# Kernel optimization log

Measured on AMD Instinct MI355X. Metric: run time of the kernel, lower is better.

## Reference

```python
import jax, jax.numpy as jnp
import numpy as np

EPS = 1e-5
K = 20
THRESH = 0.5

def _bn_relu(x, g, b, m, v):
    # eval-mode BatchNorm1d followed by ReLU
    return jax.nn.relu(g * (x - m) * jax.lax.rsqrt(v + EPS) + b)

def setup_inputs() -> dict:
    key = jax.random.key(0)
    ks = jax.random.split(key, 16)
    T, C, CI, E, NC = 16384, 256, 8, 5, 13
    B, N = 2, T // 2
    inp = {
        "f_sem": jax.random.normal(ks[0], (T, C), jnp.float32),
        "f_ins": jax.random.normal(ks[1], (T, CI), jnp.float32),
        # equal-size, sorted batch assignment (2 clouds of 8192 points)
        "batch": jnp.repeat(jnp.arange(B, dtype=jnp.int64), N),
        # semantic_adaptation_fc: Linear(C,C) + BN + ReLU
        "W_sem": jax.random.normal(ks[2], (C, C), jnp.float32) * (1.0 / np.sqrt(C)),
        "b_sem": jnp.zeros((C,), jnp.float32),
        "g_sem": jnp.ones((C,), jnp.float32),
        "beta_sem": jnp.zeros((C,), jnp.float32),
        "m_sem": jax.random.normal(ks[3], (C,), jnp.float32) * 0.1,
        "v_sem": jax.random.uniform(ks[4], (C,), jnp.float32, 0.5, 1.5),
        # inst_fc: Linear(8,C) + BN + ReLU
        "W_ins": jax.random.normal(ks[5], (CI, C), jnp.float32) * (1.0 / np.sqrt(CI)),
        "b_ins": jnp.zeros((C,), jnp.float32),
        "g_ins": jnp.ones((C,), jnp.float32),
        "beta_ins": jnp.zeros((C,), jnp.float32),
        "m_ins": jax.random.normal(ks[6], (C,), jnp.float32) * 0.1,
        "v_ins": jax.random.uniform(ks[7], (C,), jnp.float32, 0.5, 1.5),
        # instance_embedding_fc: plain Linear(C,E)
        "W_emb": jax.random.normal(ks[8], (C, E), jnp.float32) * (1.0 / np.sqrt(C)),
        "b_emb": jnp.zeros((E,), jnp.float32),
        # classifier_fc: plain Linear(C,NC)
        "W_cls": jax.random.normal(ks[9], (C, NC), jnp.float32) * (1.0 / np.sqrt(C)),
        "b_cls": jnp.zeros((NC,), jnp.float32),
    }
    return inp

def _instance_fusion(e_ins, f_sem, batch):
    # assumes sorted batch with equal-size segments (enforced by setup_inputs)
    T, C = f_sem.shape
    B = int(batch[-1]) + 1
    N = T // B
    e = e_ins.reshape(B, N, -1)
    f = f_sem.reshape(B, N, C)
    # squared Euclidean pairwise distances per cloud: [B, N, N]
    sq = jnp.sum(e * e, axis=-1)
    d2 = sq[:, :, None] + sq[:, None, :] - 2.0 * jnp.einsum("bnd,bmd->bnm", e, e)
    d2 = jnp.maximum(d2, 0.0)
    neg_vals, idx = jax.lax.top_k(-d2, K)          # k smallest distances, [B,N,K]
    within = (-neg_vals) <= THRESH * THRESH        # distance <= threshold
    self_idx = jnp.broadcast_to(jnp.arange(N)[None, :, None], idx.shape)
    col = jnp.where(within, idx, self_idx)         # fall back to self outside threshold
    neigh = jax.vmap(lambda fb, cb: fb[cb])(f, col)  # [B,N,K,C]
    return jnp.max(neigh, axis=2).reshape(T, C)      # scatter-max == max over neighbors

def reference(f_sem, f_ins, batch,
              W_sem, b_sem, g_sem, beta_sem, m_sem, v_sem,
              W_ins, b_ins, g_ins, beta_ins, m_ins, v_ins,
              W_emb, b_emb, W_cls, b_cls):
    f_sem_prime = _bn_relu(f_sem @ W_sem + b_sem, g_sem, beta_sem, m_sem, v_sem)
    f_ins_h = _bn_relu(f_ins @ W_ins + b_ins, g_ins, beta_ins, m_ins, v_ins)
    f_sins = f_ins_h + f_sem_prime
    e_ins = f_sins @ W_emb + b_emb
    f_isem = _instance_fusion(e_ins, f_sem, batch)
    p_sem = f_isem @ W_cls + b_cls
    return (p_sem, e_ins)
```

## Files before the change

kernel.cpp:

```cpp
#include <hip/hip_runtime.h>
#include <math.h>

#define T 16384
#define C 256
#define CI 8
#define EDIM 5
#define NC 13
#define NPTS 8192
#define KNN 20
#define CAP 128
#define FR 32
#define FRPB 8

typedef float f4v __attribute__((ext_vector_type(4)));
typedef _Float16 h8 __attribute__((ext_vector_type(8)));

__global__ __launch_bounds__(256) void front_kernel(
    const float* __restrict__ f_sem, const float* __restrict__ f_ins,
    const float* __restrict__ W_sem, const float* __restrict__ b_sem,
    const float* __restrict__ g_sem, const float* __restrict__ beta_sem,
    const float* __restrict__ m_sem, const float* __restrict__ v_sem,
    const float* __restrict__ W_ins, const float* __restrict__ b_ins,
    const float* __restrict__ g_ins, const float* __restrict__ beta_ins,
    const float* __restrict__ m_ins, const float* __restrict__ v_ins,
    const float* __restrict__ W_emb, const float* __restrict__ b_emb,
    float* __restrict__ eA, double* __restrict__ eD,
    float* __restrict__ out_e)
{
    __shared__ __align__(16) _Float16 sAh[FR][264];
    __shared__ __align__(16) _Float16 sAl[FR][264];
    __shared__ float bnA1[C], bnB1[C], bnA2[C], bnB2[C];
    __shared__ float weL[C][EDIM];
    __shared__ float lfi[FR][CI];
    __shared__ float sP[4][FR][EDIM];

    const int tid = threadIdx.x;
    const int rowBase = blockIdx.x * FR;

    #pragma unroll
    for (int i = 0; i < 8; i++) {
        const int idx = tid + 256 * i;
        const int g = idx * 4;
        const int row = g >> 8, k = g & 255;
        const float4 v = *(const float4*)(f_sem + (size_t)rowBase * C + g);
        const float vv[4] = {v.x, v.y, v.z, v.w};
        #pragma unroll
        for (int q = 0; q < 4; q++) {
            const _Float16 h = (_Float16)vv[q];
            sAh[row][k + q] = h;
            sAl[row][k + q] = (_Float16)(vv[q] - (float)h);
        }
    }
    {
        const int c = tid;
        const float rs1 = 1.0f / sqrtf(v_sem[c] + 1e-5f);
        const float A1 = g_sem[c] * rs1;
        bnA1[c] = A1;
        bnB1[c] = A1 * (b_sem[c] - m_sem[c]) + beta_sem[c];
        const float rs2 = 1.0f / sqrtf(v_ins[c] + 1e-5f);
        const float A2 = g_ins[c] * rs2;
        bnA2[c] = A2;
        bnB2[c] = A2 * (b_ins[c] - m_ins[c]) + beta_ins[c];
        #pragma unroll
        for (int j = 0; j < EDIM; j++) weL[c][j] = W_emb[c * EDIM + j];
    }
    if (tid < FR * CI) lfi[tid >> 3][tid & 7] = f_ins[rowBase * CI + tid];
    __syncthreads();

    const int w = tid >> 6, lane = tid & 63;
    const int r16 = lane & 15, kq = lane >> 4;
    const int n0 = 64 * w;

    f4v acc[2][4];
    #pragma unroll
    for (int mi = 0; mi < 2; mi++)
        #pragma unroll
        for (int ni = 0; ni < 4; ni++) acc[mi][ni] = (f4v){0.f, 0.f, 0.f, 0.f};

    for (int kt = 0; kt < 8; kt++) {
        const int koff = 32 * kt + 8 * kq;
        const h8 ah0 = *(const h8*)&sAh[r16][koff];
        const h8 ah1 = *(const h8*)&sAh[r16 + 16][koff];
        const h8 al0 = *(const h8*)&sAl[r16][koff];
        const h8 al1 = *(const h8*)&sAl[r16 + 16][koff];
        #pragma unroll
        for (int ni = 0; ni < 4; ni++) {
            const float* wp = W_sem + (size_t)koff * C + (n0 + 16 * ni + r16);
            float wf[8];
            #pragma unroll
            for (int j = 0; j < 8; j++) wf[j] = wp[(size_t)j * C];
            h8 bh, bl;
            #pragma unroll
            for (int j = 0; j < 8; j++) {
                const _Float16 h = (_Float16)wf[j];
                bh[j] = h;
                bl[j] = (_Float16)(wf[j] - (float)h);
            }
            acc[0][ni] = __builtin_amdgcn_mfma_f32_16x16x32_f16(ah0, bh, acc[0][ni], 0, 0, 0);
            acc[1][ni] = __builtin_amdgcn_mfma_f32_16x16x32_f16(ah1, bh, acc[1][ni], 0, 0, 0);
            acc[0][ni] = __builtin_amdgcn_mfma_f32_16x16x32_f16(al0, bh, acc[0][ni], 0, 0, 0);
            acc[1][ni] = __builtin_amdgcn_mfma_f32_16x16x32_f16(al1, bh, acc[1][ni], 0, 0, 0);
            acc[0][ni] = __builtin_amdgcn_mfma_f32_16x16x32_f16(ah0, bl, acc[0][ni], 0, 0, 0);
            acc[1][ni] = __builtin_amdgcn_mfma_f32_16x16x32_f16(ah1, bl, acc[1][ni], 0, 0, 0);
        }
    }

    f4v prow, pcol;
    {
        const f4v z = {0.f, 0.f, 0.f, 0.f};
        h8 ra, rb, ca, cb;
        #pragma unroll
        for (int j = 0; j < 8; j++) {
            ra[j] = (_Float16)(float)r16;
            rb[j] = (_Float16)((kq == 0 && j == 0) ? 1.0f : 0.0f);
            ca[j] = rb[j];
            cb[j] = ra[j];
        }
        prow = __builtin_amdgcn_mfma_f32_16x16x32_f16(ra, rb, z, 0, 0, 0);
        pcol = __builtin_amdgcn_mfma_f32_16x16x32_f16(ca, cb, z, 0, 0, 0);
    }
    const int colm = (int)pcol[0];
    int rloc[4];
    #pragma unroll
    for (int r = 0; r < 4; r++) rloc[r] = (int)prow[r];

    float p[2][4][EDIM];
    #pragma unroll
    for (int mi = 0; mi < 2; mi++)
        #pragma unroll
        for (int r = 0; r < 4; r++)
            #pragma unroll
            for (int j = 0; j < EDIM; j++) p[mi][r][j] = 0.f;

    #pragma unroll
    for (int ni = 0; ni < 4; ni++) {
        const int c = n0 + 16 * ni + colm;
        const float A1 = bnA1[c], B1 = bnB1[c];
        const float A2 = bnA2[c], B2 = bnB2[c];
        float wi[CI], we[EDIM];
        #pragma unroll
        for (int k = 0; k < CI; k++) wi[k] = W_ins[k * C + c];
        #pragma unroll
        for (int j = 0; j < EDIM; j++) we[j] = weL[c][j];
        #pragma unroll
        for (int mi = 0; mi < 2; mi++)
            #pragma unroll
            for (int r = 0; r < 4; r++) {
                const int row = 16 * mi + rloc[r];
                float x2 = 0.f;
                #pragma unroll
                for (int k = 0; k < CI; k++) x2 = fmaf(lfi[row][k], wi[k], x2);
                const float h1 = fmaxf(fmaf(A1, acc[mi][ni][r], B1), 0.f);
                const float h2 = fmaxf(fmaf(A2, x2, B2), 0.f);
                const float s = h1 + h2;
                #pragma unroll
                for (int j = 0; j < EDIM; j++) p[mi][r][j] = fmaf(s, we[j], p[mi][r][j]);
            }
    }

    #pragma unroll
    for (int off = 1; off < 16; off <<= 1)
        #pragma unroll
        for (int mi = 0; mi < 2; mi++)
            #pragma unroll
            for (int r = 0; r < 4; r++)
                #pragma unroll
                for (int j = 0; j < EDIM; j++)
                    p[mi][r][j] += __shfl_xor(p[mi][r][j], off);

    if (r16 == 0) {
        #pragma unroll
        for (int mi = 0; mi < 2; mi++)
            #pragma unroll
            for (int r = 0; r < 4; r++)
                #pragma unroll
                for (int j = 0; j < EDIM; j++)
                    sP[w][16 * mi + rloc[r]][j] = p[mi][r][j];
    }
    __syncthreads();

    if (tid < FR) {
        const int row = rowBase + tid;
        double sq = 0.0;
        #pragma unroll
        for (int j = 0; j < EDIM; j++) {
            const float s = ((sP[0][tid][j] + sP[1][tid][j]) +
                             (sP[2][tid][j] + sP[3][tid][j])) + b_emb[j];
            const double ed = (double)s;
            eD[(size_t)row * 8 + j] = ed;
            sq = fma(ed, ed, sq);
            eA[(size_t)row * 8 + j] = s;
            out_e[(size_t)row * EDIM + j] = s;
        }
        eD[(size_t)row * 8 + 5] = sq;
        eA[(size_t)row * 8 + 5] = (float)sq;
        eA[(size_t)row * 8 + 6] = 0.f;
        eA[(size_t)row * 8 + 7] = 0.f;
    }
}

__global__ __launch_bounds__(256) void stream_kernel(
    const float* __restrict__ eA,
    unsigned short* __restrict__ gcand, int* __restrict__ gcnt)
{
    __shared__ float rA[FRPB][8];
    __shared__ unsigned short cidx[FRPB][CAP];
    __shared__ int cntS[FRPB];

    const int tid = threadIdx.x;
    const int rowBase = blockIdx.x * FRPB;

    if (tid < FRPB * 8) rA[tid >> 3][tid & 7] = eA[(rowBase + (tid >> 3)) * 8 + (tid & 7)];
    if (tid < FRPB) cntS[tid] = 0;
    __syncthreads();

    const int wave = tid >> 6, lane = tid & 63;
    const int cbase = (rowBase >= NPTS) ? NPTS : 0;

    float re[FRPB][5], thrb[FRPB];
    #pragma unroll
    for (int r = 0; r < FRPB; r++) {
        #pragma unroll
        for (int q = 0; q < 5; q++) re[r][q] = rA[r][q];
        thrb[r] = (rA[r][5] - 0.251f) * 0.5f;
    }

    const int cstart = wave * (NPTS / 4);
    for (int cb = cstart; cb < cstart + NPTS / 4; cb += 128) {
        const int j0 = cbase + cb + lane;
        const float4 ea0 = *(const float4*)(eA + (size_t)j0 * 8);
        const float2 eb0 = *(const float2*)(eA + (size_t)j0 * 8 + 4);
        const float4 ea1 = *(const float4*)(eA + (size_t)(j0 + 64) * 8);
        const float2 eb1 = *(const float2*)(eA + (size_t)(j0 + 64) * 8 + 4);
        const float hs0 = 0.5f * eb0.y, hs1 = 0.5f * eb1.y;
        #pragma unroll
        for (int r = 0; r < FRPB; r++) {
            float dot = re[r][0] * ea0.x;
            dot = fmaf(re[r][1], ea0.y, dot); dot = fmaf(re[r][2], ea0.z, dot);
            dot = fmaf(re[r][3], ea0.w, dot); dot = fmaf(re[r][4], eb0.x, dot);
            const bool rec = dot >= (thrb[r] + hs0);
            const unsigned long long m = __ballot(rec);
            if (m) {
                int base;
                if (lane == 0) base = atomicAdd(&cntS[r], (int)__popcll(m));
                base = __shfl(base, 0);
                const int pre = __builtin_amdgcn_mbcnt_hi(
                    (unsigned int)(m >> 32),
                    __builtin_amdgcn_mbcnt_lo((unsigned int)m, 0u));
                const int pos = base + pre;
                if (rec && pos < CAP) cidx[r][pos] = (unsigned short)(cb + lane);
            }
        }
        #pragma unroll
        for (int r = 0; r < FRPB; r++) {
            float dot = re[r][0] * ea1.x;
            dot = fmaf(re[r][1], ea1.y, dot); dot = fmaf(re[r][2], ea1.z, dot);
            dot = fmaf(re[r][3], ea1.w, dot); dot = fmaf(re[r][4], eb1.x, dot);
            const bool rec = dot >= (thrb[r] + hs1);
            const unsigned long long m = __ballot(rec);
            if (m) {
                int base;
                if (lane == 0) base = atomicAdd(&cntS[r], (int)__popcll(m));
                base = __shfl(base, 0);
                const int pre = __builtin_amdgcn_mbcnt_hi(
                    (unsigned int)(m >> 32),
                    __builtin_amdgcn_mbcnt_lo((unsigned int)m, 0u));
                const int pos = base + pre;
                if (rec && pos < CAP) cidx[r][pos] = (unsigned short)(cb + 64 + lane);
            }
        }
    }
    __syncthreads();

    {
        const unsigned int* src = (const unsigned int*)cidx;
        unsigned int* dst = (unsigned int*)(gcand + (size_t)rowBase * CAP);
        dst[tid] = src[tid];
        dst[tid + 256] = src[tid + 256];
        if (tid < FRPB) gcnt[rowBase + tid] = cntS[tid];
    }
}

__device__ __attribute__((noinline)) float4 rescan_topk(
    const float* __restrict__ eA, const float* __restrict__ f_sem,
    const float* __restrict__ reRow, int cbase, int lane)
{
    float re0 = reRow[0], re1 = reRow[1], re2 = reRow[2];
    float re3 = reRow[3], re4 = reRow[4], sqF = reRow[5];
    float4 mx = make_float4(-3.4e38f, -3.4e38f, -3.4e38f, -3.4e38f);
    long long last = -1;
    for (int sel = 0; sel < KNN; sel++) {
        long long best = 0x7fffffffffffffffLL;
        for (int cb = 0; cb < NPTS; cb += 64) {
            const int j = cbase + cb + lane;
            const float4 ea = *(const float4*)(eA + (size_t)j * 8);
            const float2 eb = *(const float2*)(eA + (size_t)j * 8 + 4);
            float dot = re0 * ea.x;
            dot = fmaf(re1, ea.y, dot); dot = fmaf(re2, ea.z, dot);
            dot = fmaf(re3, ea.w, dot); dot = fmaf(re4, eb.x, dot);
            const float d2 = fmaxf((sqF + eb.y) - 2.f * dot, 0.f);
            long long key = (((long long)__float_as_uint(d2)) << 32)
                            | (unsigned int)(cb + lane);
            if (key <= last) key = 0x7fffffffffffffffLL;
            if (key < best) best = key;
        }
        #pragma unroll
        for (int off = 32; off; off >>= 1) {
            const long long o = __shfl_xor(best, off);
            if (o < best) best = o;
        }
        last = best;
        const int idx = (int)(best & 0xffffffffLL);
        const float4 fv = *(const float4*)(f_sem + (size_t)(cbase + idx) * C + lane * 4);
        mx.x = fmaxf(mx.x, fv.x); mx.y = fmaxf(mx.y, fv.y);
        mx.z = fmaxf(mx.z, fv.z); mx.w = fmaxf(mx.w, fv.w);
    }
    return mx;
}

__global__ __launch_bounds__(256) void resolve_kernel(
    const float* __restrict__ eA, const double* __restrict__ eD,
    const float* __restrict__ f_sem,
    const unsigned short* __restrict__ gcand, const int* __restrict__ gcnt,
    const float* __restrict__ W_cls, const float* __restrict__ b_cls,
    float* __restrict__ out_p)
{
    __shared__ float wc[C * NC];
    __shared__ float bc[NC];
    __shared__ float rA[FRPB][8];
    __shared__ double rD[FRPB][6];
    __shared__ unsigned short memL[FRPB][24];
    __shared__ int nlS[FRPB];

    const int tid = threadIdx.x;
    const int rowBase = blockIdx.x * FRPB;

    for (int i = tid; i < C * NC; i += 256) wc[i] = W_cls[i];
    if (tid < NC) bc[tid] = b_cls[tid];
    if (tid < FRPB * 8) rA[tid >> 3][tid & 7] = eA[(rowBase + (tid >> 3)) * 8 + (tid & 7)];
    if (tid < FRPB * 6) rD[tid / 6][tid % 6] = eD[(rowBase + tid / 6) * 8 + tid % 6];
    __syncthreads();

    const int wave = tid >> 6, lane = tid & 63;
    const int cbase = (rowBase >= NPTS) ? NPTS : 0;
    const int lr0 = 2 * wave, lr1 = lr0 + 1;

    #pragma unroll 1
    for (int rr = 0; rr < 2; rr++) {
        const int lr = lr0 + rr;
        const int row = rowBase + lr;
        const int n_rec = gcnt[row];
        const double* rd = rD[lr];
        const unsigned short* cand = gcand + (size_t)row * CAP;

        if (n_rec <= CAP) {
            unsigned long long key0 = ~0ull, key1 = ~0ull;
            int id0 = 0x7fffffff, id1 = 0x7fffffff;
            bool mem0 = false, mem1 = false;
            if (lane < n_rec) {
                id0 = (int)cand[lane];
                const double* ep = eD + (size_t)(cbase + id0) * 8;
                double dotd = 0.0;
                #pragma unroll
                for (int q = 0; q < 5; q++) dotd = fma(rd[q], ep[q], dotd);
                double d2 = fmax((rd[5] + ep[5]) - 2.0 * dotd, 0.0);
                mem0 = (d2 <= 0.25);
                key0 = (unsigned long long)__double_as_longlong(d2);
            }
            if (lane + 64 < n_rec) {
                id1 = (int)cand[lane + 64];
                const double* ep = eD + (size_t)(cbase + id1) * 8;
                double dotd = 0.0;
                #pragma unroll
                for (int q = 0; q < 5; q++) dotd = fma(rd[q], ep[q], dotd);
                double d2 = fmax((rd[5] + ep[5]) - 2.0 * dotd, 0.0);
                mem1 = (d2 <= 0.25);
                key1 = (unsigned long long)__double_as_longlong(d2);
            }
            const unsigned long long b0 = __ballot(mem0), b1 = __ballot(mem1);
            const int n = (int)__popcll(b0) + (int)__popcll(b1);

            if (n <= KNN) {
                if (mem0) {
                    const int pos = (int)__builtin_amdgcn_mbcnt_hi(
                        (unsigned int)(b0 >> 32),
                        __builtin_amdgcn_mbcnt_lo((unsigned int)b0, 0u));
                    memL[lr][pos] = (unsigned short)id0;
                }
                if (mem1) {
                    const int pos = (int)__popcll(b0) +
                        (int)__builtin_amdgcn_mbcnt_hi(
                            (unsigned int)(b1 >> 32),
                            __builtin_amdgcn_mbcnt_lo((unsigned int)b1, 0u));
                    memL[lr][pos] = (unsigned short)id1;
                }
                if (lane == 0) nlS[lr] = n;
            } else {
                if (!mem0) key0 = ~0ull;
                if (!mem1) key1 = ~0ull;
                for (int sel = 0; sel < KNN; sel++) {
                    const bool t = (key0 < key1) || (key0 == key1 && id0 < id1);
                    unsigned long long bk = t ? key0 : key1;
                    int bi = t ? id0 : id1;
                    #pragma unroll
                    for (int off = 32; off; off >>= 1) {
                        const unsigned long long ok = __shfl_xor(bk, off);
                        const int oi = __shfl_xor(bi, off);
                        if (ok < bk || (ok == bk && oi < bi)) { bk = ok; bi = oi; }
                    }
                    if (key0 == bk && id0 == bi) key0 = ~0ull;
                    else if (key1 == bk && id1 == bi) key1 = ~0ull;
                    if (lane == 0) memL[lr][sel] = (unsigned short)bi;
                }
                if (lane == 0) nlS[lr] = KNN;
            }
        } else {
            if (lane == 0) { memL[lr][0] = 0; nlS[lr] = -1; }
        }
    }

    const int s0 = nlS[lr0], s1 = nlS[lr1];
    const bool fb0 = (s0 < 0), fb1 = (s1 < 0);
    const int n0 = fb0 ? 1 : s0, n1 = fb1 ? 1 : s1;
    float4 mx0 = make_float4(-3.4e38f, -3.4e38f, -3.4e38f, -3.4e38f);
    float4 mx1 = mx0;
    const int nmax = (n0 > n1) ? n0 : n1;
    for (int k = 0; k < nmax; k += 4) {
        const int a0 = (int)memL[lr0][(k     < n0) ? k     : n0 - 1];
        const int a1 = (int)memL[lr0][(k + 1 < n0) ? k + 1 : n0 - 1];
        const int a2 = (int)memL[lr0][(k + 2 < n0) ? k + 2 : n0 - 1];
        const int a3 = (int)memL[lr0][(k + 3 < n0) ? k + 3 : n0 - 1];
        const int c0 = (int)memL[lr1][(k     < n1) ? k     : n1 - 1];
        const int c1 = (int)memL[lr1][(k + 1 < n1) ? k + 1 : n1 - 1];
        const int c2 = (int)memL[lr1][(k + 2 < n1) ? k + 2 : n1 - 1];
        const int c3 = (int)memL[lr1][(k + 3 < n1) ? k + 3 : n1 - 1];
        const float4 f0 = *(const float4*)(f_sem + (size_t)(cbase + a0) * C + lane * 4);
        const float4 f1 = *(const float4*)(f_sem + (size_t)(cbase + a1) * C + lane * 4);
        const float4 f2 = *(const float4*)(f_sem + (size_t)(cbase + a2) * C + lane * 4);
        const float4 f3 = *(const float4*)(f_sem + (size_t)(cbase + a3) * C + lane * 4);
        const float4 g0 = *(const float4*)(f_sem + (size_t)(cbase + c0) * C + lane * 4);
        const float4 g1 = *(const float4*)(f_sem + (size_t)(cbase + c1) * C + lane * 4);
        const float4 g2 = *(const float4*)(f_sem + (size_t)(cbase + c2) * C + lane * 4);
        const float4 g3 = *(const float4*)(f_sem + (size_t)(cbase + c3) * C + lane * 4);
        mx0.x = fmaxf(fmaxf(fmaxf(mx0.x, f0.x), fmaxf(f1.x, f2.x)), f3.x);
        mx0.y = fmaxf(fmaxf(fmaxf(mx0.y, f0.y), fmaxf(f1.y, f2.y)), f3.y);
        mx0.z = fmaxf(fmaxf(fmaxf(mx0.z, f0.z), fmaxf(f1.z, f2.z)), f3.z);
        mx0.w = fmaxf(fmaxf(fmaxf(mx0.w, f0.w), fmaxf(f1.w, f2.w)), f3.w);
        mx1.x = fmaxf(fmaxf(fmaxf(mx1.x, g0.x), fmaxf(g1.x, g2.x)), g3.x);
        mx1.y = fmaxf(fmaxf(fmaxf(mx1.y, g0.y), fmaxf(g1.y, g2.y)), g3.y);
        mx1.z = fmaxf(fmaxf(fmaxf(mx1.z, g0.z), fmaxf(g1.z, g2.z)), g3.z);
        mx1.w = fmaxf(fmaxf(fmaxf(mx1.w, g0.w), fmaxf(g1.w, g2.w)), g3.w);
    }
    if (fb0) mx0 = rescan_topk(eA, f_sem, rA[lr0], cbase, lane);
    if (fb1) mx1 = rescan_topk(eA, f_sem, rA[lr1], cbase, lane);

    #pragma unroll 1
    for (int rr = 0; rr < 2; rr++) {
        const float4 mx = rr ? mx1 : mx0;
        float p[NC];
        #pragma unroll
        for (int k = 0; k < NC; k++) p[k] = 0.f;
        const float* w0 = &wc[(4 * lane + 0) * NC];
        const float* w1 = &wc[(4 * lane + 1) * NC];
        const float* w2 = &wc[(4 * lane + 2) * NC];
        const float* w3 = &wc[(4 * lane + 3) * NC];
        #pragma unroll
        for (int k = 0; k < NC; k++)
            p[k] = fmaf(mx.x, w0[k], fmaf(mx.y, w1[k], fmaf(mx.z, w2[k], fmaf(mx.w, w3[k], p[k]))));
        #pragma unroll
        for (int off = 32; off; off >>= 1)
            #pragma unroll
            for (int k = 0; k < NC; k++) p[k] += __shfl_xor(p[k], off);
        if (lane == 0) {
            const int row = rowBase + lr0 + rr;
            #pragma unroll
            for (int k = 0; k < NC; k++) out_p[row * NC + k] = p[k] + bc[k];
        }
    }
}

extern "C" void kernel_launch(void* const* d_in, const int* in_sizes, int n_in,
                              void* d_out, int out_size, void* d_ws, size_t ws_size,
                              hipStream_t stream) {
    (void)in_sizes; (void)n_in; (void)out_size; (void)ws_size;
    const float* f_sem    = (const float*)d_in[0];
    const float* f_ins    = (const float*)d_in[1];
    const float* W_sem    = (const float*)d_in[3];
    const float* b_sem    = (const float*)d_in[4];
    const float* g_sem    = (const float*)d_in[5];
    const float* beta_sem = (const float*)d_in[6];
    const float* m_sem    = (const float*)d_in[7];
    const float* v_sem    = (const float*)d_in[8];
    const float* W_ins    = (const float*)d_in[9];
    const float* b_ins    = (const float*)d_in[10];
    const float* g_ins    = (const float*)d_in[11];
    const float* beta_ins = (const float*)d_in[12];
    const float* m_ins    = (const float*)d_in[13];
    const float* v_ins    = (const float*)d_in[14];
    const float* W_emb    = (const float*)d_in[15];
    const float* b_emb    = (const float*)d_in[16];
    const float* W_cls    = (const float*)d_in[17];
    const float* b_cls    = (const float*)d_in[18];
    float* outp = (float*)d_out;

    char* ws = (char*)d_ws;
    float*  eA = (float*)ws;
    double* eD = (double*)(ws + (size_t)T * 8 * 4);
    int*    gcnt  = (int*)(ws + (size_t)T * 8 * 12);
    unsigned short* gcand =
        (unsigned short*)(ws + (size_t)T * 8 * 12 + T * 4);

    front_kernel<<<T / FR, 256, 0, stream>>>(
        f_sem, f_ins, W_sem, b_sem, g_sem, beta_sem, m_sem, v_sem,
        W_ins, b_ins, g_ins, beta_ins, m_ins, v_ins, W_emb, b_emb,
        eA, eD, outp + T * NC);
    stream_kernel<<<T / FRPB, 256, 0, stream>>>(eA, gcand, gcnt);
    resolve_kernel<<<T / FRPB, 256, 0, stream>>>(
        eA, eD, f_sem, gcand, gcnt, W_cls, b_cls, outp);
}
```

Before: 200.9 us.

## Fuse candidate streaming into resolve kernel and gather half-precision semantic features

```diff
diff --git a/kernel.cpp b/kernel.cpp
--- a/kernel.cpp
+++ b/kernel.cpp
@@ -14,6 +14,7 @@
 
 typedef float f4v __attribute__((ext_vector_type(4)));
 typedef _Float16 h8 __attribute__((ext_vector_type(8)));
+typedef _Float16 h4v __attribute__((ext_vector_type(4)));
 
 __global__ __launch_bounds__(256) void front_kernel(
     const float* __restrict__ f_sem, const float* __restrict__ f_ins,
@@ -25,7 +26,7 @@
     const float* __restrict__ m_ins, const float* __restrict__ v_ins,
     const float* __restrict__ W_emb, const float* __restrict__ b_emb,
     float* __restrict__ eA, double* __restrict__ eD,
-    float* __restrict__ out_e)
+    float* __restrict__ out_e, _Float16* __restrict__ fsem_h)
 {
     __shared__ __align__(16) _Float16 sAh[FR][264];
     __shared__ __align__(16) _Float16 sAl[FR][264];
@@ -44,12 +45,16 @@
         const int row = g >> 8, k = g & 255;
         const float4 v = *(const float4*)(f_sem + (size_t)rowBase * C + g);
         const float vv[4] = {v.x, v.y, v.z, v.w};
+        h4v hv;
         #pragma unroll
         for (int q = 0; q < 4; q++) {
             const _Float16 h = (_Float16)vv[q];
             sAh[row][k + q] = h;
             sAl[row][k + q] = (_Float16)(vv[q] - (float)h);
-        }
+            hv[q] = h;
+        }
+        if (fsem_h)
+            *(h4v*)(fsem_h + (size_t)(rowBase + row) * C + k) = hv;
     }
     {
         const int c = tid;
@@ -196,88 +201,6 @@
         eA[(size_t)row * 8 + 5] = (float)sq;
         eA[(size_t)row * 8 + 6] = 0.f;
         eA[(size_t)row * 8 + 7] = 0.f;
-    }
-}
-
-__global__ __launch_bounds__(256) void stream_kernel(
-    const float* __restrict__ eA,
-    unsigned short* __restrict__ gcand, int* __restrict__ gcnt)
-{
-    __shared__ float rA[FRPB][8];
-    __shared__ unsigned short cidx[FRPB][CAP];
-    __shared__ int cntS[FRPB];
-
-    const int tid = threadIdx.x;
-    const int rowBase = blockIdx.x * FRPB;
-
-    if (tid < FRPB * 8) rA[tid >> 3][tid & 7] = eA[(rowBase + (tid >> 3)) * 8 + (tid & 7)];
-    if (tid < FRPB) cntS[tid] = 0;
-    __syncthreads();
-
-    const int wave = tid >> 6, lane = tid & 63;
-    const int cbase = (rowBase >= NPTS) ? NPTS : 0;
-
-    float re[FRPB][5], thrb[FRPB];
-    #pragma unroll
-    for (int r = 0; r < FRPB; r++) {
-        #pragma unroll
-        for (int q = 0; q < 5; q++) re[r][q] = rA[r][q];
-        thrb[r] = (rA[r][5] - 0.251f) * 0.5f;
-    }
-
-    const int cstart = wave * (NPTS / 4);
-    for (int cb = cstart; cb < cstart + NPTS / 4; cb += 128) {
-        const int j0 = cbase + cb + lane;
-        const float4 ea0 = *(const float4*)(eA + (size_t)j0 * 8);
-        const float2 eb0 = *(const float2*)(eA + (size_t)j0 * 8 + 4);
-        const float4 ea1 = *(const float4*)(eA + (size_t)(j0 + 64) * 8);
-        const float2 eb1 = *(const float2*)(eA + (size_t)(j0 + 64) * 8 + 4);
-        const float hs0 = 0.5f * eb0.y, hs1 = 0.5f * eb1.y;
-        #pragma unroll
-        for (int r = 0; r < FRPB; r++) {
-            float dot = re[r][0] * ea0.x;
-            dot = fmaf(re[r][1], ea0.y, dot); dot = fmaf(re[r][2], ea0.z, dot);
-            dot = fmaf(re[r][3], ea0.w, dot); dot = fmaf(re[r][4], eb0.x, dot);
-            const bool rec = dot >= (thrb[r] + hs0);
-            const unsigned long long m = __ballot(rec);
-            if (m) {
-                int base;
-                if (lane == 0) base = atomicAdd(&cntS[r], (int)__popcll(m));
-                base = __shfl(base, 0);
-                const int pre = __builtin_amdgcn_mbcnt_hi(
-                    (unsigned int)(m >> 32),
-                    __builtin_amdgcn_mbcnt_lo((unsigned int)m, 0u));
-                const int pos = base + pre;
-                if (rec && pos < CAP) cidx[r][pos] = (unsigned short)(cb + lane);
-            }
-        }
-        #pragma unroll
-        for (int r = 0; r < FRPB; r++) {
-            float dot = re[r][0] * ea1.x;
-            dot = fmaf(re[r][1], ea1.y, dot); dot = fmaf(re[r][2], ea1.z, dot);
-            dot = fmaf(re[r][3], ea1.w, dot); dot = fmaf(re[r][4], eb1.x, dot);
-            const bool rec = dot >= (thrb[r] + hs1);
-            const unsigned long long m = __ballot(rec);
-            if (m) {
-                int base;
-                if (lane == 0) base = atomicAdd(&cntS[r], (int)__popcll(m));
-                base = __shfl(base, 0);
-                const int pre = __builtin_amdgcn_mbcnt_hi(
-                    (unsigned int)(m >> 32),
-                    __builtin_amdgcn_mbcnt_lo((unsigned int)m, 0u));
-                const int pos = base + pre;
-                if (rec && pos < CAP) cidx[r][pos] = (unsigned short)(cb + 64 + lane);
-            }
-        }
-    }
-    __syncthreads();
-
-    {
-        const unsigned int* src = (const unsigned int*)cidx;
-        unsigned int* dst = (unsigned int*)(gcand + (size_t)rowBase * CAP);
-        dst[tid] = src[tid];
-        dst[tid + 256] = src[tid + 256];
-        if (tid < FRPB) gcnt[rowBase + tid] = cntS[tid];
     }
 }
 
@@ -318,10 +241,10 @@
     return mx;
 }
 
-__global__ __launch_bounds__(256) void resolve_kernel(
+template <bool H16>
+__global__ __launch_bounds__(256) void knn_kernel(
     const float* __restrict__ eA, const double* __restrict__ eD,
-    const float* __restrict__ f_sem,
-    const unsigned short* __restrict__ gcand, const int* __restrict__ gcnt,
+    const float* __restrict__ f_sem, const _Float16* __restrict__ fsem_h,
     const float* __restrict__ W_cls, const float* __restrict__ b_cls,
     float* __restrict__ out_p)
 {
@@ -329,6 +252,8 @@
     __shared__ float bc[NC];
     __shared__ float rA[FRPB][8];
     __shared__ double rD[FRPB][6];
+    __shared__ unsigned short cidx[FRPB][CAP];
+    __shared__ int cntS[FRPB];
     __shared__ unsigned short memL[FRPB][24];
     __shared__ int nlS[FRPB];
 
@@ -339,19 +264,77 @@
     if (tid < NC) bc[tid] = b_cls[tid];
     if (tid < FRPB * 8) rA[tid >> 3][tid & 7] = eA[(rowBase + (tid >> 3)) * 8 + (tid & 7)];
     if (tid < FRPB * 6) rD[tid / 6][tid % 6] = eD[(rowBase + tid / 6) * 8 + tid % 6];
+    if (tid < FRPB) cntS[tid] = 0;
     __syncthreads();
 
     const int wave = tid >> 6, lane = tid & 63;
     const int cbase = (rowBase >= NPTS) ? NPTS : 0;
+
+    {
+        float re[FRPB][5], thrb[FRPB];
+        #pragma unroll
+        for (int r = 0; r < FRPB; r++) {
+            #pragma unroll
+            for (int q = 0; q < 5; q++) re[r][q] = rA[r][q];
+            thrb[r] = (rA[r][5] - 0.251f) * 0.5f;
+        }
+
+        const int cstart = wave * (NPTS / 4);
+        for (int cb = cstart; cb < cstart + NPTS / 4; cb += 128) {
+            const int j0 = cbase + cb + lane;
+            const float4 ea0 = *(const float4*)(eA + (size_t)j0 * 8);
+            const float2 eb0 = *(const float2*)(eA + (size_t)j0 * 8 + 4);
+            const float4 ea1 = *(const float4*)(eA + (size_t)(j0 + 64) * 8);
+            const float2 eb1 = *(const float2*)(eA + (size_t)(j0 + 64) * 8 + 4);
+            const float hs0 = 0.5f * eb0.y, hs1 = 0.5f * eb1.y;
+            #pragma unroll
+            for (int r = 0; r < FRPB; r++) {
+                float dot = re[r][0] * ea0.x;
+                dot = fmaf(re[r][1], ea0.y, dot); dot = fmaf(re[r][2], ea0.z, dot);
+                dot = fmaf(re[r][3], ea0.w, dot); dot = fmaf(re[r][4], eb0.x, dot);
+                const bool rec = dot >= (thrb[r] + hs0);
+                const unsigned long long m = __ballot(rec);
+                if (m) {
+                    int base;
+                    if (lane == 0) base = atomicAdd(&cntS[r], (int)__popcll(m));
+                    base = __shfl(base, 0);
+                    const int pre = __builtin_amdgcn_mbcnt_hi(
+                        (unsigned int)(m >> 32),
+                        __builtin_amdgcn_mbcnt_lo((unsigned int)m, 0u));
+                    const int pos = base + pre;
+                    if (rec && pos < CAP) cidx[r][pos] = (unsigned short)(cb + lane);
+                }
+            }
+            #pragma unroll
+            for (int r = 0; r < FRPB; r++) {
+                float dot = re[r][0] * ea1.x;
+                dot = fmaf(re[r][1], ea1.y, dot); dot = fmaf(re[r][2], ea1.z, dot);
+                dot = fmaf(re[r][3], ea1.w, dot); dot = fmaf(re[r][4], eb1.x, dot);
+                const bool rec = dot >= (thrb[r] + hs1);
+                const unsigned long long m = __ballot(rec);
+                if (m) {
+                    int base;
+                    if (lane == 0) base = atomicAdd(&cntS[r], (int)__popcll(m));
+                    base = __shfl(base, 0);
+                    const int pre = __builtin_amdgcn_mbcnt_hi(
+                        (unsigned int)(m >> 32),
+                        __builtin_amdgcn_mbcnt_lo((unsigned int)m, 0u));
+                    const int pos = base + pre;
+                    if (rec && pos < CAP) cidx[r][pos] = (unsigned short)(cb + 64 + lane);
+                }
+            }
+        }
+    }
+    __syncthreads();
+
     const int lr0 = 2 * wave, lr1 = lr0 + 1;
 
     #pragma unroll 1
     for (int rr = 0; rr < 2; rr++) {
         const int lr = lr0 + rr;
-        const int row = rowBase + lr;
-        const int n_rec = gcnt[row];
+        const int n_rec = cntS[lr];
         const double* rd = rD[lr];
-        const unsigned short* cand = gcand + (size_t)row * CAP;
+        const unsigned short* cand = cidx[lr];
 
         if (n_rec <= CAP) {
             unsigned long long key0 = ~0ull, key1 = ~0ull;
@@ -425,31 +408,60 @@
     float4 mx0 = make_float4(-3.4e38f, -3.4e38f, -3.4e38f, -3.4e38f);
     float4 mx1 = mx0;
     const int nmax = (n0 > n1) ? n0 : n1;
-    for (int k = 0; k < nmax; k += 4) {
-        const int a0 = (int)memL[lr0][(k     < n0) ? k     : n0 - 1];
-        const int a1 = (int)memL[lr0][(k + 1 < n0) ? k + 1 : n0 - 1];
-        const int a2 = (int)memL[lr0][(k + 2 < n0) ? k + 2 : n0 - 1];
-        const int a3 = (int)memL[lr0][(k + 3 < n0) ? k + 3 : n0 - 1];
-        const int c0 = (int)memL[lr1][(k     < n1) ? k     : n1 - 1];
-        const int c1 = (int)memL[lr1][(k + 1 < n1) ? k + 1 : n1 - 1];
-        const int c2 = (int)memL[lr1][(k + 2 < n1) ? k + 2 : n1 - 1];
-        const int c3 = (int)memL[lr1][(k + 3 < n1) ? k + 3 : n1 - 1];
-        const float4 f0 = *(const float4*)(f_sem + (size_t)(cbase + a0) * C + lane * 4);
-        const float4 f1 = *(const float4*)(f_sem + (size_t)(cbase + a1) * C + lane * 4);
-        const float4 f2 = *(const float4*)(f_sem + (size_t)(cbase + a2) * C + lane * 4);
-        const float4 f3 = *(const float4*)(f_sem + (size_t)(cbase + a3) * C + lane * 4);
-        const float4 g0 = *(const float4*)(f_sem + (size_t)(cbase + c0) * C + lane * 4);
-        const float4 g1 = *(const float4*)(f_sem + (size_t)(cbase + c1) * C + lane * 4);
-        const float4 g2 = *(const float4*)(f_sem + (size_t)(cbase + c2) * C + lane * 4);
-        const float4 g3 = *(const float4*)(f_sem + (size_t)(cbase + c3) * C + lane * 4);
-        mx0.x = fmaxf(fmaxf(fmaxf(mx0.x, f0.x), fmaxf(f1.x, f2.x)), f3.x);
-        mx0.y = fmaxf(fmaxf(fmaxf(mx0.y, f0.y), fmaxf(f1.y, f2.y)), f3.y);
-        mx0.z = fmaxf(fmaxf(fmaxf(mx0.z, f0.z), fmaxf(f1.z, f2.z)), f3.z);
-        mx0.w = fmaxf(fmaxf(fmaxf(mx0.w, f0.w), fmaxf(f1.w, f2.w)), f3.w);
-        mx1.x = fmaxf(fmaxf(fmaxf(mx1.x, g0.x), fmaxf(g1.x, g2.x)), g3.x);
-        mx1.y = fmaxf(fmaxf(fmaxf(mx1.y, g0.y), fmaxf(g1.y, g2.y)), g3.y);
-        mx1.z = fmaxf(fmaxf(fmaxf(mx1.z, g0.z), fmaxf(g1.z, g2.z)), g3.z);
-        mx1.w = fmaxf(fmaxf(fmaxf(mx1.w, g0.w), fmaxf(g1.w, g2.w)), g3.w);
+
+    if (H16) {
+        for (int k = 0; k < nmax; k += 8) {
+            int a[8], c[8];
+            #pragma unroll
+            for (int i = 0; i < 8; i++) {
+                a[i] = (int)memL[lr0][(k + i < n0) ? k + i : n0 - 1];
+                c[i] = (int)memL[lr1][(k + i < n1) ? k + i : n1 - 1];
+            }
+            h4v fa[8], fc[8];
+            #pragma unroll
+            for (int i = 0; i < 8; i++) {
+                fa[i] = *(const h4v*)(fsem_h + (size_t)(cbase + a[i]) * C + lane * 4);
+                fc[i] = *(const h4v*)(fsem_h + (size_t)(cbase + c[i]) * C + lane * 4);
+            }
+            #pragma unroll
+            for (int i = 0; i < 8; i++) {
+                mx0.x = fmaxf(mx0.x, (float)fa[i][0]);
+                mx0.y = fmaxf(mx0.y, (float)fa[i][1]);
+                mx0.z = fmaxf(mx0.z, (float)fa[i][2]);
+                mx0.w = fmaxf(mx0.w, (float)fa[i][3]);
+                mx1.x = fmaxf(mx1.x, (float)fc[i][0]);
+                mx1.y = fmaxf(mx1.y, (float)fc[i][1]);
+                mx1.z = fmaxf(mx1.z, (float)fc[i][2]);
+                mx1.w = fmaxf(mx1.w, (float)fc[i][3]);
+            }
+        }
+    } else {
+        for (int k = 0; k < nmax; k += 4) {
+            const int a0 = (int)memL[lr0][(k     < n0) ? k     : n0 - 1];
+            const int a1 = (int)memL[lr0][(k + 1 < n0) ? k + 1 : n0 - 1];
+            const int a2 = (int)memL[lr0][(k + 2 < n0) ? k + 2 : n0 - 1];
+            const int a3 = (int)memL[lr0][(k + 3 < n0) ? k + 3 : n0 - 1];
+            const int c0 = (int)memL[lr1][(k     < n1) ? k     : n1 - 1];
+            const int c1 = (int)memL[lr1][(k + 1 < n1) ? k + 1 : n1 - 1];
+            const int c2 = (int)memL[lr1][(k + 2 < n1) ? k + 2 : n1 - 1];
+            const int c3 = (int)memL[lr1][(k + 3 < n1) ? k + 3 : n1 - 1];
+            const float4 f0 = *(const float4*)(f_sem + (size_t)(cbase + a0) * C + lane * 4);
+            const float4 f1 = *(const float4*)(f_sem + (size_t)(cbase + a1) * C + lane * 4);
+            const float4 f2 = *(const float4*)(f_sem + (size_t)(cbase + a2) * C + lane * 4);
+            const float4 f3 = *(const float4*)(f_sem + (size_t)(cbase + a3) * C + lane * 4);
+            const float4 g0 = *(const float4*)(f_sem + (size_t)(cbase + c0) * C + lane * 4);
+            const float4 g1 = *(const float4*)(f_sem + (size_t)(cbase + c1) * C + lane * 4);
+            const float4 g2 = *(const float4*)(f_sem + (size_t)(cbase + c2) * C + lane * 4);
+            const float4 g3 = *(const float4*)(f_sem + (size_t)(cbase + c3) * C + lane * 4);
+            mx0.x = fmaxf(fmaxf(fmaxf(mx0.x, f0.x), fmaxf(f1.x, f2.x)), f3.x);
+            mx0.y = fmaxf(fmaxf(fmaxf(mx0.y, f0.y), fmaxf(f1.y, f2.y)), f3.y);
+            mx0.z = fmaxf(fmaxf(fmaxf(mx0.z, f0.z), fmaxf(f1.z, f2.z)), f3.z);
+            mx0.w = fmaxf(fmaxf(fmaxf(mx0.w, f0.w), fmaxf(f1.w, f2.w)), f3.w);
+            mx1.x = fmaxf(fmaxf(fmaxf(mx1.x, g0.x), fmaxf(g1.x, g2.x)), g3.x);
+            mx1.y = fmaxf(fmaxf(fmaxf(mx1.y, g0.y), fmaxf(g1.y, g2.y)), g3.y);
+            mx1.z = fmaxf(fmaxf(fmaxf(mx1.z, g0.z), fmaxf(g1.z, g2.z)), g3.z);
+            mx1.w = fmaxf(fmaxf(fmaxf(mx1.w, g0.w), fmaxf(g1.w, g2.w)), g3.w);
+        }
     }
     if (fb0) mx0 = rescan_topk(eA, f_sem, rA[lr0], cbase, lane);
     if (fb1) mx1 = rescan_topk(eA, f_sem, rA[lr1], cbase, lane);
@@ -482,7 +494,7 @@
 extern "C" void kernel_launch(void* const* d_in, const int* in_sizes, int n_in,
                               void* d_out, int out_size, void* d_ws, size_t ws_size,
                               hipStream_t stream) {
-    (void)in_sizes; (void)n_in; (void)out_size; (void)ws_size;
+    (void)in_sizes; (void)n_in; (void)out_size;
     const float* f_sem    = (const float*)d_in[0];
     const float* f_ins    = (const float*)d_in[1];
     const float* W_sem    = (const float*)d_in[3];
@@ -504,17 +516,21 @@
     float* outp = (float*)d_out;
 
     char* ws = (char*)d_ws;
-    float*  eA = (float*)ws;
-    double* eD = (double*)(ws + (size_t)T * 8 * 4);
-    int*    gcnt  = (int*)(ws + (size_t)T * 8 * 12);
-    unsigned short* gcand =
-        (unsigned short*)(ws + (size_t)T * 8 * 12 + T * 4);
+    float*    eA     = (float*)ws;
+    double*   eD     = (double*)(ws + (size_t)T * 8 * 4);
+    _Float16* fsem_h = (_Float16*)(ws + (size_t)T * 8 * 12);
+
+    const size_t need = (size_t)T * 8 * 12 + (size_t)T * C * 2;
+    const bool h16 = (ws_size >= need);
 
     front_kernel<<<T / FR, 256, 0, stream>>>(
         f_sem, f_ins, W_sem, b_sem, g_sem, beta_sem, m_sem, v_sem,
         W_ins, b_ins, g_ins, beta_ins, m_ins, v_ins, W_emb, b_emb,
-        eA, eD, outp + T * NC);
-    stream_kernel<<<T / FRPB, 256, 0, stream>>>(eA, gcand, gcnt);
-    resolve_kernel<<<T / FRPB, 256, 0, stream>>>(
-        eA, eD, f_sem, gcand, gcnt, W_cls, b_cls, outp);
+        eA, eD, outp + T * NC, h16 ? fsem_h : (_Float16*)nullptr);
+    if (h16)
+        knn_kernel<true><<<T / FRPB, 256, 0, stream>>>(
+            eA, eD, f_sem, fsem_h, W_cls, b_cls, outp);
+    else
+        knn_kernel<false><<<T / FRPB, 256, 0, stream>>>(
+            eA, eD, f_sem, (const _Float16*)nullptr, W_cls, b_cls, outp);
 }
```

New measurement: 210.1 us. +4.6%, slower.

## Fuse candidate stream and resolve kernels into one kNN kernel with rank selection

Applied to the files above, without the earlier changes.

```diff
diff --git a/kernel.cpp b/kernel.cpp
--- a/kernel.cpp
+++ b/kernel.cpp
@@ -8,7 +8,7 @@
 #define NC 13
 #define NPTS 8192
 #define KNN 20
-#define CAP 128
+#define CAP 256
 #define FR 32
 #define FRPB 8
 
@@ -196,88 +196,6 @@
         eA[(size_t)row * 8 + 5] = (float)sq;
         eA[(size_t)row * 8 + 6] = 0.f;
         eA[(size_t)row * 8 + 7] = 0.f;
-    }
-}
-
-__global__ __launch_bounds__(256) void stream_kernel(
-    const float* __restrict__ eA,
-    unsigned short* __restrict__ gcand, int* __restrict__ gcnt)
-{
-    __shared__ float rA[FRPB][8];
-    __shared__ unsigned short cidx[FRPB][CAP];
-    __shared__ int cntS[FRPB];
-
-    const int tid = threadIdx.x;
-    const int rowBase = blockIdx.x * FRPB;
-
-    if (tid < FRPB * 8) rA[tid >> 3][tid & 7] = eA[(rowBase + (tid >> 3)) * 8 + (tid & 7)];
-    if (tid < FRPB) cntS[tid] = 0;
-    __syncthreads();
-
-    const int wave = tid >> 6, lane = tid & 63;
-    const int cbase = (rowBase >= NPTS) ? NPTS : 0;
-
-    float re[FRPB][5], thrb[FRPB];
-    #pragma unroll
-    for (int r = 0; r < FRPB; r++) {
-        #pragma unroll
-        for (int q = 0; q < 5; q++) re[r][q] = rA[r][q];
-        thrb[r] = (rA[r][5] - 0.251f) * 0.5f;
-    }
-
-    const int cstart = wave * (NPTS / 4);
-    for (int cb = cstart; cb < cstart + NPTS / 4; cb += 128) {
-        const int j0 = cbase + cb + lane;
-        const float4 ea0 = *(const float4*)(eA + (size_t)j0 * 8);
-        const float2 eb0 = *(const float2*)(eA + (size_t)j0 * 8 + 4);
-        const float4 ea1 = *(const float4*)(eA + (size_t)(j0 + 64) * 8);
-        const float2 eb1 = *(const float2*)(eA + (size_t)(j0 + 64) * 8 + 4);
-        const float hs0 = 0.5f * eb0.y, hs1 = 0.5f * eb1.y;
-        #pragma unroll
-        for (int r = 0; r < FRPB; r++) {
-            float dot = re[r][0] * ea0.x;
-            dot = fmaf(re[r][1], ea0.y, dot); dot = fmaf(re[r][2], ea0.z, dot);
-            dot = fmaf(re[r][3], ea0.w, dot); dot = fmaf(re[r][4], eb0.x, dot);
-            const bool rec = dot >= (thrb[r] + hs0);
-            const unsigned long long m = __ballot(rec);
-            if (m) {
-                int base;
-                if (lane == 0) base = atomicAdd(&cntS[r], (int)__popcll(m));
-                base = __shfl(base, 0);
-                const int pre = __builtin_amdgcn_mbcnt_hi(
-                    (unsigned int)(m >> 32),
-                    __builtin_amdgcn_mbcnt_lo((unsigned int)m, 0u));
-                const int pos = base + pre;
-                if (rec && pos < CAP) cidx[r][pos] = (unsigned short)(cb + lane);
-            }
-        }
-        #pragma unroll
-        for (int r = 0; r < FRPB; r++) {
-            float dot = re[r][0] * ea1.x;
-            dot = fmaf(re[r][1], ea1.y, dot); dot = fmaf(re[r][2], ea1.z, dot);
-            dot = fmaf(re[r][3], ea1.w, dot); dot = fmaf(re[r][4], eb1.x, dot);
-            const bool rec = dot >= (thrb[r] + hs1);
-            const unsigned long long m = __ballot(rec);
-            if (m) {
-                int base;
-                if (lane == 0) base = atomicAdd(&cntS[r], (int)__popcll(m));
-                base = __shfl(base, 0);
-                const int pre = __builtin_amdgcn_mbcnt_hi(
-                    (unsigned int)(m >> 32),
-                    __builtin_amdgcn_mbcnt_lo((unsigned int)m, 0u));
-                const int pos = base + pre;
-                if (rec && pos < CAP) cidx[r][pos] = (unsigned short)(cb + 64 + lane);
-            }
-        }
-    }
-    __syncthreads();
-
-    {
-        const unsigned int* src = (const unsigned int*)cidx;
-        unsigned int* dst = (unsigned int*)(gcand + (size_t)rowBase * CAP);
-        dst[tid] = src[tid];
-        dst[tid + 256] = src[tid + 256];
-        if (tid < FRPB) gcnt[rowBase + tid] = cntS[tid];
     }
 }
 
@@ -318,102 +236,139 @@
     return mx;
 }
 
-__global__ __launch_bounds__(256) void resolve_kernel(
+__global__ __launch_bounds__(256) void knn_kernel(
     const float* __restrict__ eA, const double* __restrict__ eD,
     const float* __restrict__ f_sem,
-    const unsigned short* __restrict__ gcand, const int* __restrict__ gcnt,
     const float* __restrict__ W_cls, const float* __restrict__ b_cls,
     float* __restrict__ out_p)
 {
-    __shared__ float wc[C * NC];
-    __shared__ float bc[NC];
     __shared__ float rA[FRPB][8];
     __shared__ double rD[FRPB][6];
+    __shared__ unsigned short cidx[FRPB][CAP];
+    __shared__ unsigned long long kD[FRPB][CAP];
+    __shared__ int cntS[FRPB];
     __shared__ unsigned short memL[FRPB][24];
     __shared__ int nlS[FRPB];
 
     const int tid = threadIdx.x;
     const int rowBase = blockIdx.x * FRPB;
 
-    for (int i = tid; i < C * NC; i += 256) wc[i] = W_cls[i];
-    if (tid < NC) bc[tid] = b_cls[tid];
     if (tid < FRPB * 8) rA[tid >> 3][tid & 7] = eA[(rowBase + (tid >> 3)) * 8 + (tid & 7)];
     if (tid < FRPB * 6) rD[tid / 6][tid % 6] = eD[(rowBase + tid / 6) * 8 + tid % 6];
+    if (tid < FRPB) cntS[tid] = 0;
     __syncthreads();
 
     const int wave = tid >> 6, lane = tid & 63;
     const int cbase = (rowBase >= NPTS) ? NPTS : 0;
+
+    {
+        float re[FRPB][5], thrb[FRPB];
+        #pragma unroll
+        for (int r = 0; r < FRPB; r++) {
+            #pragma unroll
+            for (int q = 0; q < 5; q++) re[r][q] = rA[r][q];
+            thrb[r] = (rA[r][5] - 0.251f) * 0.5f;
+        }
+
+        const int cstart = wave * (NPTS / 4);
+        for (int cb = cstart; cb < cstart + NPTS / 4; cb += 128) {
+            const int j0 = cbase + cb + lane;
+            const float4 ea0 = *(const float4*)(eA + (size_t)j0 * 8);
+            const float2 eb0 = *(const float2*)(eA + (size_t)j0 * 8 + 4);
+            const float4 ea1 = *(const float4*)(eA + (size_t)(j0 + 64) * 8);
+            const float2 eb1 = *(const float2*)(eA + (size_t)(j0 + 64) * 8 + 4);
+            const float hs0 = 0.5f * eb0.y, hs1 = 0.5f * eb1.y;
+            #pragma unroll
+            for (int r = 0; r < FRPB; r++) {
+                float dot = re[r][0] * ea0.x;
+                dot = fmaf(re[r][1], ea0.y, dot); dot = fmaf(re[r][2], ea0.z, dot);
+                dot = fmaf(re[r][3], ea0.w, dot); dot = fmaf(re[r][4], eb0.x, dot);
+                const bool rec = dot >= (thrb[r] + hs0);
+                const unsigned long long m = __ballot(rec);
+                if (m) {
+                    int base;
+                    if (lane == 0) base = atomicAdd(&cntS[r], (int)__popcll(m));
+                    base = __shfl(base, 0);
+                    const int pre = __builtin_amdgcn_mbcnt_hi(
+                        (unsigned int)(m >> 32),
+                        __builtin_amdgcn_mbcnt_lo((unsigned int)m, 0u));
+                    const int pos = base + pre;
+                    if (rec && pos < CAP) cidx[r][pos] = (unsigned short)(cb + lane);
+                }
+            }
+            #pragma unroll
+            for (int r = 0; r < FRPB; r++) {
+                float dot = re[r][0] * ea1.x;
+                dot = fmaf(re[r][1], ea1.y, dot); dot = fmaf(re[r][2], ea1.z, dot);
+                dot = fmaf(re[r][3], ea1.w, dot); dot = fmaf(re[r][4], eb1.x, dot);
+                const bool rec = dot >= (thrb[r] + hs1);
+                const unsigned long long m = __ballot(rec);
+                if (m) {
+                    int base;
+                    if (lane == 0) base = atomicAdd(&cntS[r], (int)__popcll(m));
+                    base = __shfl(base, 0);
+                    const int pre = __builtin_amdgcn_mbcnt_hi(
+                        (unsigned int)(m >> 32),
+                        __builtin_amdgcn_mbcnt_lo((unsigned int)m, 0u));
+                    const int pos = base + pre;
+                    if (rec && pos < CAP) cidx[r][pos] = (unsigned short)(cb + 64 + lane);
+                }
+            }
+        }
+    }
+    __syncthreads();
+
     const int lr0 = 2 * wave, lr1 = lr0 + 1;
 
     #pragma unroll 1
     for (int rr = 0; rr < 2; rr++) {
         const int lr = lr0 + rr;
-        const int row = rowBase + lr;
-        const int n_rec = gcnt[row];
+        const int cnt = cntS[lr];
         const double* rd = rD[lr];
-        const unsigned short* cand = gcand + (size_t)row * CAP;
-
-        if (n_rec <= CAP) {
-            unsigned long long key0 = ~0ull, key1 = ~0ull;
-            int id0 = 0x7fffffff, id1 = 0x7fffffff;
-            bool mem0 = false, mem1 = false;
-            if (lane < n_rec) {
-                id0 = (int)cand[lane];
-                const double* ep = eD + (size_t)(cbase + id0) * 8;
-                double dotd = 0.0;
+
+        if (cnt <= CAP) {
+            unsigned long long myk[4];
+            int myid[4];
+            bool mem[4];
+            #pragma unroll
+            for (int q = 0; q < 4; q++) {
+                const int i = lane + 64 * q;
+                myk[q] = ~0ull; myid[q] = -1; mem[q] = false;
+                if (i < cnt) {
+                    const int id = (int)cidx[lr][i];
+                    const double* ep = eD + (size_t)(cbase + id) * 8;
+                    double dotd = 0.0;
+                    #pragma unroll
+                    for (int qq = 0; qq < 5; qq++) dotd = fma(rd[qq], ep[qq], dotd);
+                    const double d2 = fmax((rd[5] + ep[5]) - 2.0 * dotd, 0.0);
+                    const unsigned long long ku =
+                        (((unsigned long long)__double_as_longlong(d2)) & ~0x1FFFull)
+                        | (unsigned long long)id;
+                    kD[lr][i] = ku;
+                    myk[q] = ku; myid[q] = id;
+                    mem[q] = (d2 <= 0.25);
+                }
+            }
+            int rank[4] = {0, 0, 0, 0};
+            for (int j = 0; j < cnt; j++) {
+                const unsigned long long kj = kD[lr][j];
                 #pragma unroll
-                for (int q = 0; q < 5; q++) dotd = fma(rd[q], ep[q], dotd);
-                double d2 = fmax((rd[5] + ep[5]) - 2.0 * dotd, 0.0);
-                mem0 = (d2 <= 0.25);
-                key0 = (unsigned long long)__double_as_longlong(d2);
-            }
-            if (lane + 64 < n_rec) {
-                id1 = (int)cand[lane + 64];
-                const double* ep = eD + (size_t)(cbase + id1) * 8;
-                double dotd = 0.0;
-                #pragma unroll
-                for (int q = 0; q < 5; q++) dotd = fma(rd[q], ep[q], dotd);
-                double d2 = fmax((rd[5] + ep[5]) - 2.0 * dotd, 0.0);
-                mem1 = (d2 <= 0.25);
-                key1 = (unsigned long long)__double_as_longlong(d2);
-            }
-            const unsigned long long b0 = __ballot(mem0), b1 = __ballot(mem1);
-            const int n = (int)__popcll(b0) + (int)__popcll(b1);
-
-            if (n <= KNN) {
-                if (mem0) {
-                    const int pos = (int)__builtin_amdgcn_mbcnt_hi(
-                        (unsigned int)(b0 >> 32),
-                        __builtin_amdgcn_mbcnt_lo((unsigned int)b0, 0u));
-                    memL[lr][pos] = (unsigned short)id0;
+                for (int q = 0; q < 4; q++) rank[q] += (kj < myk[q]) ? 1 : 0;
+            }
+            int base = 0;
+            #pragma unroll
+            for (int q = 0; q < 4; q++) {
+                const bool sel = mem[q] && (rank[q] < KNN);
+                const unsigned long long b = __ballot(sel);
+                if (sel) {
+                    const int pos = base + (int)__builtin_amdgcn_mbcnt_hi(
+                        (unsigned int)(b >> 32),
+                        __builtin_amdgcn_mbcnt_lo((unsigned int)b, 0u));
+                    memL[lr][pos] = (unsigned short)myid[q];
                 }
-                if (mem1) {
-                    const int pos = (int)__popcll(b0) +
-                        (int)__builtin_amdgcn_mbcnt_hi(
-                            (unsigned int)(b1 >> 32),
-                            __builtin_amdgcn_mbcnt_lo((unsigned int)b1, 0u));
-                    memL[lr][pos] = (unsigned short)id1;
-                }
-                if (lane == 0) nlS[lr] = n;
-            } else {
-                if (!mem0) key0 = ~0ull;
-                if (!mem1) key1 = ~0ull;
-                for (int sel = 0; sel < KNN; sel++) {
-                    const bool t = (key0 < key1) || (key0 == key1 && id0 < id1);
-                    unsigned long long bk = t ? key0 : key1;
-                    int bi = t ? id0 : id1;
-                    #pragma unroll
-                    for (int off = 32; off; off >>= 1) {
-                        const unsigned long long ok = __shfl_xor(bk, off);
-                        const int oi = __shfl_xor(bi, off);
-                        if (ok < bk || (ok == bk && oi < bi)) { bk = ok; bi = oi; }
-                    }
-                    if (key0 == bk && id0 == bi) key0 = ~0ull;
-                    else if (key1 == bk && id1 == bi) key1 = ~0ull;
-                    if (lane == 0) memL[lr][sel] = (unsigned short)bi;
-                }
-                if (lane == 0) nlS[lr] = KNN;
-            }
+                base += (int)__popcll(b);
+            }
+            if (lane == 0) nlS[lr] = base;
         } else {
             if (lane == 0) { memL[lr][0] = 0; nlS[lr] = -1; }
         }
@@ -460,10 +415,10 @@
         float p[NC];
         #pragma unroll
         for (int k = 0; k < NC; k++) p[k] = 0.f;
-        const float* w0 = &wc[(4 * lane + 0) * NC];
-        const float* w1 = &wc[(4 * lane + 1) * NC];
-        const float* w2 = &wc[(4 * lane + 2) * NC];
-        const float* w3 = &wc[(4 * lane + 3) * NC];
+        const float* w0 = W_cls + (4 * lane + 0) * NC;
+        const float* w1 = W_cls + (4 * lane + 1) * NC;
+        const float* w2 = W_cls + (4 * lane + 2) * NC;
+        const float* w3 = W_cls + (4 * lane + 3) * NC;
         #pragma unroll
         for (int k = 0; k < NC; k++)
             p[k] = fmaf(mx.x, w0[k], fmaf(mx.y, w1[k], fmaf(mx.z, w2[k], fmaf(mx.w, w3[k], p[k]))));
@@ -474,7 +429,7 @@
         if (lane == 0) {
             const int row = rowBase + lr0 + rr;
             #pragma unroll
-            for (int k = 0; k < NC; k++) out_p[row * NC + k] = p[k] + bc[k];
+            for (int k = 0; k < NC; k++) out_p[row * NC + k] = p[k] + b_cls[k];
         }
     }
 }
@@ -506,15 +461,11 @@
     char* ws = (char*)d_ws;
     float*  eA = (float*)ws;
     double* eD = (double*)(ws + (size_t)T * 8 * 4);
-    int*    gcnt  = (int*)(ws + (size_t)T * 8 * 12);
-    unsigned short* gcand =
-        (unsigned short*)(ws + (size_t)T * 8 * 12 + T * 4);
 
     front_kernel<<<T / FR, 256, 0, stream>>>(
         f_sem, f_ins, W_sem, b_sem, g_sem, beta_sem, m_sem, v_sem,
         W_ins, b_ins, g_ins, beta_ins, m_ins, v_ins, W_emb, b_emb,
         eA, eD, outp + T * NC);
-    stream_kernel<<<T / FRPB, 256, 0, stream>>>(eA, gcand, gcnt);
-    resolve_kernel<<<T / FRPB, 256, 0, stream>>>(
-        eA, eD, f_sem, gcand, gcnt, W_cls, b_cls, outp);
+    knn_kernel<<<T / FRPB, 256, 0, stream>>>(
+        eA, eD, f_sem, W_cls, b_cls, outp);
 }
```

Result: faster. 167.6 us (-16.6%).
